# Performance work log

Measured on AMD Instinct MI355X. Metric: run time of the kernel, lower is better.

The kernel has to match this reference:

```python
import jax, jax.numpy as jnp
import numpy as np
import math

DIM = 32
K = 10
B = 2048


def _perm_weights(dim, order):
    # weight = 1 / (number of distinct orderings of the index tuple), so each
    # unique symmetric moment is counted once (reconstruction of GaussMoments.moment_weights)
    idx = np.indices((dim,) * order).reshape(order, -1)
    s = np.sort(idx, axis=0)
    prod = np.ones(s.shape[1], dtype=np.float64)
    count = np.ones(s.shape[1], dtype=np.float64)
    for p in range(1, order):
        count = np.where(s[p] == s[p - 1], count + 1.0, 1.0)
        prod *= count
    return (prod / math.factorial(order)).reshape((dim,) * order).astype(np.float32)


def _gauss_targets(dim):
    # Joint moments of a standard multivariate normal (Isserlis' theorem)
    I = np.eye(dim, dtype=np.float32)
    m1 = np.zeros((dim,), np.float32)
    m2 = I
    m3 = np.zeros((dim,) * 3, np.float32)
    m4 = (np.einsum('ij,kl->ijkl', I, I) + np.einsum('ik,jl->ijkl', I, I)
          + np.einsum('il,jk->ijkl', I, I)).astype(np.float32)
    return m1, m2, m3, m4


def _compress(m, c_add, p, c_sub):
    return jnp.sign(jnp.sign(m) + 0.1) * (jnp.power(jnp.abs(m) + c_add, p) - c_sub)


def setup_inputs() -> dict:
    key = jax.random.key(0)
    k1, k2, k3 = jax.random.split(key, 3)
    return {
        'embedding': jax.random.normal(k1, (B, DIM), jnp.float32),
        'centers': jax.random.normal(k2, (K, DIM), jnp.float32),
        'logits': jax.random.normal(k3, (B, K), jnp.float32),
    }


def reference(embedding, centers, logits):
    dim = embedding.shape[-1]
    k = logits.shape[-1]
    dt = embedding.dtype
    w1 = jnp.asarray(_perm_weights(dim, 1))
    w2 = jnp.asarray(_perm_weights(dim, 2))
    w3 = jnp.asarray(_perm_weights(dim, 3))
    w4 = jnp.asarray(_perm_weights(dim, 4))
    t1, t2, t3, t4 = [jnp.asarray(t) for t in _gauss_targets(dim)]

    onehot = jax.nn.one_hot(jnp.argmax(logits, axis=-1), k, dtype=dt)  # (B,K)
    diff = embedding[:, None, :] - centers[None, :, :]                 # (B,K,D)
    diff_oh = diff * onehot[:, :, None]                                # (B,K,D)
    cw = jnp.sum(onehot, axis=0)                                       # (K,)
    cnt = cw[:, None] + 1e-7

    m1 = jnp.sum(diff_oh, axis=0) / cnt                                # (K,D)
    outer2 = jnp.einsum('bki,bkj->bkij', diff_oh, diff_oh)             # (B,K,D,D)
    m2 = jnp.sum(outer2, axis=0) / cnt[:, :, None]                     # (K,D,D)
    # NOTE: original code does NOT divide moment3/moment4 by counts -- kept faithful
    m3 = jnp.einsum('bkij,bkl->kijl', outer2, diff_oh)                 # (K,D,D,D)
    m4 = jnp.einsum('bkij,bklm->kijlm', outer2, outer2)                # (K,D,D,D,D)

    m2 = _compress(m2, 0.25, 0.5, 0.5)
    t2c = _compress(t2, 0.25, 0.5, 0.5)
    m3 = _compress(m3, 0.19245008973, 0.3333333333, 0.57735026919)
    t3c = _compress(t3, 0.19245008973, 0.3333333333, 0.57735026919)
    m4 = _compress(m4, 0.15749013123, 0.25, 0.62996052494)
    t4c = _compress(t4, 0.15749013123, 0.25, 0.62996052494)

    cwn = cw / jnp.sum(cw)
    off_diag = 1.0 - jnp.eye(dim, dtype=dt)

    p1 = jnp.sum(cwn[:, None] * w1[None] * (m1 - t1[None]) ** 2)
    w2m = cwn[:, None, None] * w2[None] * off_diag[None]
    p2 = jnp.sum(w2m * (m2 - t2c[None]) ** 2)
    p3 = jnp.sum(cwn[:, None, None, None] * w3[None] * (m3 - t3c[None]) ** 2)
    w4m = cwn[:, None, None, None, None] * w4[None] * off_diag[None, None, None]
    p4 = jnp.sum(w4m * (m4 - t4c[None]) ** 2)

    return 1.0 * p1 + 0.5 * p2 + 0.25 * p3 + 0.125 * p4
```

## Files before the change

kernel.cpp:

```cpp
#include <hip/hip_runtime.h>
#include <math.h>

#define B_N 2048
#define DIM 32
#define K_N 10
#define NP  528
#define NCOLP 640
#define TILE 128
#define NT 5
#define NBLK (NT*NT*K_N)

typedef __attribute__((ext_vector_type(8))) short bf16x8;
typedef __attribute__((ext_vector_type(4))) float f32x4;

#define WS_LOSS 0
#define WS_CTR  1
#define WS_CWP  16
#define WS_KB   160

__device__ __forceinline__ float c2f(float x) {
  float r = sqrtf(fabsf(x) + 0.25f) - 0.5f;
  return (x >= 0.f) ? r : -r;
}
__device__ __forceinline__ float c3f(float x) {
  float v = fabsf(x) + 0.19245008973f;
  float r = exp2f(log2f(v) * 0.33333333333f) - 0.57735026919f;
  return (x >= 0.f) ? r : -r;
}
__device__ __forceinline__ float c4f(float x) {
  float r = sqrtf(sqrtf(fabsf(x) + 0.15749013123f)) - 0.62996052494f;
  return (x >= 0.f) ? r : -r;
}
#define T4C1 (sqrtf(sqrtf(1.f + 0.15749013123f)) - 0.62996052494f)

__device__ __forceinline__ void decode_col(int g, int& u, int& v) {
  if (g < NP) {
    int j = (int)((sqrtf(8.f * (float)g + 1.f) - 1.f) * 0.5f);
    while (j * (j + 1) / 2 > g) --j;
    while ((j + 1) * (j + 2) / 2 <= g) ++j;
    u = g - j * (j + 1) / 2; v = j;
  } else if (g < 560) { u = g - NP; v = 32; }
  else if (g == 560)  { u = 32; v = 32; }
  else                { u = 33; v = 33; }
}

__device__ __forceinline__ unsigned short f2bf(float f) {
  unsigned u = __builtin_bit_cast(unsigned, f);
  return (unsigned short)((u + 0x7FFFu + ((u >> 16) & 1u)) >> 16);
}

__global__ __launch_bounds__(256) void k_assign(const float* __restrict__ logits,
                                                int* __restrict__ kb,
                                                int* __restrict__ cwp) {
  __shared__ int scw[K_N];
  const int t = threadIdx.x;
  if (t < K_N) scw[t] = 0;
  __syncthreads();
  int b = blockIdx.x * 256 + t;
  const float* l = logits + (size_t)b * K_N;
  float best = l[0]; int bi = 0;
  #pragma unroll
  for (int k = 1; k < K_N; ++k) { float v = l[k]; if (v > best) { best = v; bi = k; } }
  kb[b] = bi;
  atomicAdd(&scw[bi], 1);
  __syncthreads();
  if (t < K_N) cwp[blockIdx.x * 16 + t] = scw[t];
}

__global__ __launch_bounds__(1024) void k_main(const float* __restrict__ emb,
                                               const float* __restrict__ cen,
                                               const int* __restrict__ kb,
                                               const int* __restrict__ cwp,
                                               float* __restrict__ lossAcc,
                                               int* __restrict__ ctr,
                                               float* __restrict__ out) {
  const int k  = blockIdx.z;
  const int Pt = blockIdx.y, Qt = blockIdx.x;
  const int t  = threadIdx.x;
  const int wid = t >> 6, lane = t & 63;
  const int wr = wid >> 2, wc = wid & 3;
  const int lr = lane & 15, kg = lane >> 4;

  __shared__ unsigned char tI0[NCOLP], tI1[NCOLP];
  __shared__ unsigned short rl[B_N];
  __shared__ __align__(16) float sd[32][36];
  __shared__ __align__(16) unsigned short tiles[2][4][TILE][8];
  __shared__ float scen[DIM];
  __shared__ int wcs[16];
  __shared__ float sred[16];

  if (t < NCOLP) {
    int u, v; decode_col(t, u, v);
    tI0[t] = (unsigned char)u; tI1[t] = (unsigned char)v;
  }
  if (t < DIM) scen[t] = cen[k * DIM + t];
  int nb = 0;
  #pragma unroll
  for (int p = 0; p < 8; ++p) nb += cwp[p * 16 + k];
  __syncthreads();

  int base = 0;
  #pragma unroll
  for (int rd = 0; rd < 2; ++rd) {
    int e = rd * 1024 + t;
    bool f = (kb[e] == k);
    unsigned long long m = __ballot(f);
    int wpre = __popcll(m & ((1ull << lane) - 1ull));
    if (lane == 0) wcs[wid] = __popcll(m);
    __syncthreads();
    int off = base;
    for (int q = 0; q < wid; ++q) off += wcs[q];
    if (f) rl[off + wpre] = (unsigned short)e;
    int tot = 0;
    #pragma unroll
    for (int q = 0; q < 16; ++q) tot += wcs[q];
    base += tot;
    __syncthreads();
  }

  f32x4 acc[2][2];
  {
    f32x4 z = {0.f, 0.f, 0.f, 0.f};
    acc[0][0] = z; acc[0][1] = z; acc[1][0] = z; acc[1][1] = z;
  }

  const float4* e4 = reinterpret_cast<const float4*>(emb);

  for (int cb = 0; cb < nb; cb += 32) {
    if (t < 256) {
      int r = t >> 3, part = t & 7;
      int idx = cb + r;
      float4 v = make_float4(0.f, 0.f, 0.f, 0.f);
      if (idx < nb) {
        int g = rl[idx];
        float4 e = e4[g * 8 + part];
        v = make_float4(e.x - scen[part * 4], e.y - scen[part * 4 + 1],
                        e.z - scen[part * 4 + 2], e.w - scen[part * 4 + 3]);
      }
      *reinterpret_cast<float4*>(&sd[r][part * 4]) = v;
      if (part == 0) { sd[r][32] = (idx < nb) ? 1.f : 0.f; sd[r][33] = 0.f; }
    }
    __syncthreads();
    {
      int side = t >> 9;
      int rem  = t & 511;
      int ch = rem >> 7, col = rem & 127;
      int gcol = (side ? Qt : Pt) * TILE + col;
      int u = tI0[gcol], v = tI1[gcol];
      bf16x8 pk;
      #pragma unroll
      for (int e = 0; e < 8; ++e)
        pk[e] = (short)f2bf(sd[ch * 8 + e][u] * sd[ch * 8 + e][v]);
      *reinterpret_cast<bf16x8*>(&tiles[side][ch][col][0]) = pk;
    }
    __syncthreads();
    bf16x8 a[2], b[2];
    #pragma unroll
    for (int f = 0; f < 2; ++f) {
      a[f] = *reinterpret_cast<const bf16x8*>(&tiles[0][kg][wr * 32 + f * 16 + lr][0]);
      b[f] = *reinterpret_cast<const bf16x8*>(&tiles[1][kg][wc * 32 + f * 16 + lr][0]);
    }
    #pragma unroll
    for (int fa = 0; fa < 2; ++fa)
      #pragma unroll
      for (int fc = 0; fc < 2; ++fc)
        acc[fa][fc] = __builtin_amdgcn_mfma_f32_16x16x32_bf16(a[fa], b[fc], acc[fa][fc], 0, 0, 0);
    __syncthreads();
  }

  const int pb = Pt * TILE + wr * 32;
  const int qb = Qt * TILE + wc * 32;
  const float inv_cnt = 1.f / ((float)nb + 1e-7f);
  float sum = 0.f;
  #pragma unroll
  for (int fa = 0; fa < 2; ++fa) {
    #pragma unroll
    for (int r = 0; r < 4; ++r) {
      const int P = pb + fa * 16 + kg * 4 + r;
      const int i = tI0[P], j = tI1[P];
      #pragma unroll
      for (int fc = 0; fc < 2; ++fc) {
        const int Q = qb + fc * 16 + lr;
        const int li = tI0[Q], mi = tI1[Q];
        const float g = acc[fa][fc][r];
        if (P < NP) {
          if (Q < NP) {
            int s0 = min(i, li), x1 = max(i, li), x2 = min(j, mi), s3 = max(j, mi);
            int s1 = min(x1, x2), s2 = max(x1, x2);
            bool e01 = (s0 == s1), e12 = (s1 == s2), e23 = (s2 == s3);
            float wgt, tgt = 0.f;
            if (e01 && e12 && e23)                 wgt = 0.f;
            else if (e01 && e23)                   { wgt = 2.f / 9.f; tgt = T4C1; }
            else if ((e01 && e12) || (e12 && e23)) wgt = 0.25f;
            else if (e01 || e12 || e23)            wgt = 5.f / 24.f;
            else                                   wgt = 1.f / 6.f;
            float d = c4f(g) - tgt;
            sum += 0.125f * wgt * d * d;
          } else if (Q < 560) {
            if (Q - NP >= j) { float d = c3f(g); sum += 0.25f * d * d; }
          } else if (Q == 560) {
            if (i < j) { float d = c2f(g * inv_cnt); sum += 0.5f * d * d; }
          }
        } else if (P < 560 && Q == 560) {
          float m1 = g * inv_cnt;
          sum += m1 * m1;
        }
      }
    }
  }

  #pragma unroll
  for (int off = 32; off > 0; off >>= 1) sum += __shfl_down(sum, off, 64);
  if (lane == 0) sred[wid] = sum;
  __syncthreads();
  if (t == 0) {
    float s = 0.f;
    #pragma unroll
    for (int q = 0; q < 16; ++q) s += sred[q];
    atomicAdd(lossAcc, s * ((float)nb * (1.f / (float)B_N)));
    __threadfence();
    if (atomicAdd(ctr, 1) == NBLK - 1) out[0] = atomicAdd(lossAcc, 0.f);
  }
}

extern "C" void kernel_launch(void* const* d_in, const int* in_sizes, int n_in,
                              void* d_out, int out_size, void* d_ws, size_t ws_size,
                              hipStream_t stream) {
  const float* emb = (const float*)d_in[0];
  const float* cen = (const float*)d_in[1];
  const float* lg  = (const float*)d_in[2];
  float* out = (float*)d_out;
  int*   wsi = (int*)d_ws;
  float* wsf = (float*)d_ws;

  int*   kb    = wsi + WS_KB;
  int*   cwp   = wsi + WS_CWP;
  float* lossA = wsf + WS_LOSS;
  int*   ctr   = wsi + WS_CTR;

  (void)hipMemsetAsync(d_ws, 0, 64 * 4, stream);
  k_assign<<<B_N / 256, 256, 0, stream>>>(lg, kb, cwp);
  k_main  <<<dim3(NT, NT, K_N), 1024, 0, stream>>>(emb, cen, kb, cwp, lossA, ctr, out);
}
```

Baseline: 31.30 us.

## Fuse argmax assignment into main kernel, double chunk size, prefetch embeddings

Removes the separate assignment kernel: every block of the main kernel now computes the argmax of all 2048 logit rows itself into shared memory and derives the cluster count from the ballot compaction. The batch chunk per iteration grows from 32 to 64 rows, so each iteration issues twice as many MFMAs per barrier round. The next chunk's embedding rows are register-prefetched while the current tile is built. This saves one kernel launch and halves loop iterations and syncs, but every one of the 250 blocks redundantly reads the whole 80 KB logits array.

After: 28.88 us. 1.08x faster.

```diff
diff --git a/kernel.cpp b/kernel.cpp
--- a/kernel.cpp
+++ b/kernel.cpp
@@ -9,14 +9,13 @@
 #define TILE 128
 #define NT 5
 #define NBLK (NT*NT*K_N)
+#define CH 64
 
 typedef __attribute__((ext_vector_type(8))) short bf16x8;
 typedef __attribute__((ext_vector_type(4))) float f32x4;
 
 #define WS_LOSS 0
 #define WS_CTR  1
-#define WS_CWP  16
-#define WS_KB   160
 
 __device__ __forceinline__ float c2f(float x) {
   float r = sqrtf(fabsf(x) + 0.25f) - 0.5f;
@@ -49,28 +48,9 @@
   return (unsigned short)((u + 0x7FFFu + ((u >> 16) & 1u)) >> 16);
 }
 
-__global__ __launch_bounds__(256) void k_assign(const float* __restrict__ logits,
-                                                int* __restrict__ kb,
-                                                int* __restrict__ cwp) {
-  __shared__ int scw[K_N];
-  const int t = threadIdx.x;
-  if (t < K_N) scw[t] = 0;
-  __syncthreads();
-  int b = blockIdx.x * 256 + t;
-  const float* l = logits + (size_t)b * K_N;
-  float best = l[0]; int bi = 0;
-  #pragma unroll
-  for (int k = 1; k < K_N; ++k) { float v = l[k]; if (v > best) { best = v; bi = k; } }
-  kb[b] = bi;
-  atomicAdd(&scw[bi], 1);
-  __syncthreads();
-  if (t < K_N) cwp[blockIdx.x * 16 + t] = scw[t];
-}
-
 __global__ __launch_bounds__(1024) void k_main(const float* __restrict__ emb,
                                                const float* __restrict__ cen,
-                                               const int* __restrict__ kb,
-                                               const int* __restrict__ cwp,
+                                               const float* __restrict__ lg,
                                                float* __restrict__ lossAcc,
                                                int* __restrict__ ctr,
                                                float* __restrict__ out) {
@@ -82,9 +62,10 @@
   const int lr = lane & 15, kg = lane >> 4;
 
   __shared__ unsigned char tI0[NCOLP], tI1[NCOLP];
+  __shared__ short skb[B_N];
   __shared__ unsigned short rl[B_N];
-  __shared__ __align__(16) float sd[32][36];
-  __shared__ __align__(16) unsigned short tiles[2][4][TILE][8];
+  __shared__ __align__(16) float sd[CH][36];
+  __shared__ __align__(16) unsigned short tiles[2][8][TILE][8];
   __shared__ float scen[DIM];
   __shared__ int wcs[16];
   __shared__ float sred[16];
@@ -94,27 +75,33 @@
     tI0[t] = (unsigned char)u; tI1[t] = (unsigned char)v;
   }
   if (t < DIM) scen[t] = cen[k * DIM + t];
+  #pragma unroll
+  for (int rd = 0; rd < 2; ++rd) {
+    int b = rd * 1024 + t;
+    const float* l = lg + (size_t)b * K_N;
+    float best = l[0]; int bi = 0;
+    #pragma unroll
+    for (int q = 1; q < K_N; ++q) { float v = l[q]; if (v > best) { best = v; bi = q; } }
+    skb[b] = (short)bi;
+  }
+  __syncthreads();
+
   int nb = 0;
-  #pragma unroll
-  for (int p = 0; p < 8; ++p) nb += cwp[p * 16 + k];
-  __syncthreads();
-
-  int base = 0;
   #pragma unroll
   for (int rd = 0; rd < 2; ++rd) {
     int e = rd * 1024 + t;
-    bool f = (kb[e] == k);
+    bool f = (skb[e] == (short)k);
     unsigned long long m = __ballot(f);
     int wpre = __popcll(m & ((1ull << lane) - 1ull));
     if (lane == 0) wcs[wid] = __popcll(m);
     __syncthreads();
-    int off = base;
+    int off = nb;
     for (int q = 0; q < wid; ++q) off += wcs[q];
     if (f) rl[off + wpre] = (unsigned short)e;
     int tot = 0;
     #pragma unroll
     for (int q = 0; q < 16; ++q) tot += wcs[q];
-    base += tot;
+    nb += tot;
     __syncthreads();
   }
 
@@ -125,25 +112,41 @@
   }
 
   const float4* e4 = reinterpret_cast<const float4*>(emb);
-
-  for (int cb = 0; cb < nb; cb += 32) {
-    if (t < 256) {
-      int r = t >> 3, part = t & 7;
-      int idx = cb + r;
-      float4 v = make_float4(0.f, 0.f, 0.f, 0.f);
-      if (idx < nb) {
-        int g = rl[idx];
-        float4 e = e4[g * 8 + part];
-        v = make_float4(e.x - scen[part * 4], e.y - scen[part * 4 + 1],
-                        e.z - scen[part * 4 + 2], e.w - scen[part * 4 + 3]);
+  const int gr = t >> 3, gpart = t & 7;
+
+  float4 pf = make_float4(0.f, 0.f, 0.f, 0.f);
+  bool pvalid = false;
+  if (t < 512) {
+    int idx = gr;
+    pvalid = (idx < nb);
+    if (pvalid) {
+      float4 e = e4[rl[idx] * 8 + gpart];
+      pf = make_float4(e.x - scen[gpart * 4], e.y - scen[gpart * 4 + 1],
+                       e.z - scen[gpart * 4 + 2], e.w - scen[gpart * 4 + 3]);
+    }
+  }
+
+  for (int cb = 0; cb < nb; cb += CH) {
+    if (t < 512) {
+      *reinterpret_cast<float4*>(&sd[gr][gpart * 4]) = pf;
+      if (gpart == 0) { sd[gr][32] = pvalid ? 1.f : 0.f; sd[gr][33] = 0.f; }
+    }
+    __syncthreads();
+    if (t < 512) {
+      int idx = cb + CH + gr;
+      pvalid = (idx < nb);
+      pf = make_float4(0.f, 0.f, 0.f, 0.f);
+      if (pvalid) {
+        float4 e = e4[rl[idx] * 8 + gpart];
+        pf = make_float4(e.x - scen[gpart * 4], e.y - scen[gpart * 4 + 1],
+                         e.z - scen[gpart * 4 + 2], e.w - scen[gpart * 4 + 3]);
       }
-      *reinterpret_cast<float4*>(&sd[r][part * 4]) = v;
-      if (part == 0) { sd[r][32] = (idx < nb) ? 1.f : 0.f; sd[r][33] = 0.f; }
-    }
-    __syncthreads();
-    {
-      int side = t >> 9;
-      int rem  = t & 511;
+    }
+    #pragma unroll
+    for (int uu = 0; uu < 2; ++uu) {
+      int unit = t + uu * 1024;
+      int side = unit >> 10;
+      int rem  = unit & 1023;
       int ch = rem >> 7, col = rem & 127;
       int gcol = (side ? Qt : Pt) * TILE + col;
       int u = tI0[gcol], v = tI1[gcol];
@@ -154,17 +157,20 @@
       *reinterpret_cast<bf16x8*>(&tiles[side][ch][col][0]) = pk;
     }
     __syncthreads();
-    bf16x8 a[2], b[2];
-    #pragma unroll
-    for (int f = 0; f < 2; ++f) {
-      a[f] = *reinterpret_cast<const bf16x8*>(&tiles[0][kg][wr * 32 + f * 16 + lr][0]);
-      b[f] = *reinterpret_cast<const bf16x8*>(&tiles[1][kg][wc * 32 + f * 16 + lr][0]);
-    }
-    #pragma unroll
-    for (int fa = 0; fa < 2; ++fa)
-      #pragma unroll
-      for (int fc = 0; fc < 2; ++fc)
-        acc[fa][fc] = __builtin_amdgcn_mfma_f32_16x16x32_bf16(a[fa], b[fc], acc[fa][fc], 0, 0, 0);
+    #pragma unroll
+    for (int s = 0; s < 2; ++s) {
+      bf16x8 a[2], b[2];
+      #pragma unroll
+      for (int f = 0; f < 2; ++f) {
+        a[f] = *reinterpret_cast<const bf16x8*>(&tiles[0][s * 4 + kg][wr * 32 + f * 16 + lr][0]);
+        b[f] = *reinterpret_cast<const bf16x8*>(&tiles[1][s * 4 + kg][wc * 32 + f * 16 + lr][0]);
+      }
+      #pragma unroll
+      for (int fa = 0; fa < 2; ++fa)
+        #pragma unroll
+        for (int fc = 0; fc < 2; ++fc)
+          acc[fa][fc] = __builtin_amdgcn_mfma_f32_16x16x32_bf16(a[fa], b[fc], acc[fa][fc], 0, 0, 0);
+    }
     __syncthreads();
   }
 
@@ -230,15 +236,12 @@
   const float* cen = (const float*)d_in[1];
   const float* lg  = (const float*)d_in[2];
   float* out = (float*)d_out;
+  float* wsf = (float*)d_ws;
   int*   wsi = (int*)d_ws;
-  float* wsf = (float*)d_ws;
-
-  int*   kb    = wsi + WS_KB;
-  int*   cwp   = wsi + WS_CWP;
+
   float* lossA = wsf + WS_LOSS;
   int*   ctr   = wsi + WS_CTR;
 
   (void)hipMemsetAsync(d_ws, 0, 64 * 4, stream);
-  k_assign<<<B_N / 256, 256, 0, stream>>>(lg, kb, cwp);
-  k_main  <<<dim3(NT, NT, K_N), 1024, 0, stream>>>(emb, cen, kb, cwp, lossA, ctr, out);
-}
+  k_main<<<dim3(NT, NT, K_N), 1024, 0, stream>>>(emb, cen, lg, lossA, ctr, out);
+}
```
